# Optimization experiments

Hardware: AMD Instinct MI355X
Metric: run time of the kernel (lower is better)

## Reference

```python
import jax, jax.numpy as jnp
import numpy as np
from jax import lax

B, C, Dd, Hh, Ww = 2, 256, 8, 64, 64
E, HID, TOPK = 6, 1024, 3


def setup_inputs() -> dict:
    key = jax.random.key(0)
    ks = jax.random.split(key, 8)
    return {
        "x": jax.random.normal(ks[0], (B, C, Dd, Hh, Ww), jnp.float32),
        "attention_weights": jax.random.uniform(ks[1], (B, Dd, Hh, Ww), jnp.float32),
        "gate_w": jax.random.normal(ks[2], (E, C), jnp.float32) * 0.02,
        "gate_b": jnp.zeros((E,), jnp.float32),
        "w1": jax.random.normal(ks[3], (E, HID, C), jnp.float32) * (1.0 / np.sqrt(C)),
        "b1": jnp.zeros((E, HID), jnp.float32),
        "w2": jax.random.normal(ks[4], (E, C, HID), jnp.float32) * (1.0 / np.sqrt(HID)),
        "b2": jnp.zeros((E, C), jnp.float32),
    }


def reference(x, attention_weights, gate_w, gate_b, w1, b1, w2, b2):
    b, c, d, h, w = x.shape
    n = d * h * w
    e = gate_w.shape[0]
    xt = x.reshape(b, c, n).transpose(0, 2, 1)  # [B, N, C] tokens
    # 1x1x1 gate conv == per-voxel linear
    gv = jnp.einsum('bnc,ec->bne', xt, gate_w) + gate_b  # [B, N, E]
    gv = gv * attention_weights.reshape(b, n, 1)
    gv = jax.nn.softmax(gv, axis=-1)  # softmax over experts (dim=1 in torch layout)
    top_v, top_i = lax.top_k(gv, TOPK)  # [B, N, 3]
    # scatter top-k softmax values into a zero mask (non-topk experts get 0)
    mask = jnp.sum(jax.nn.one_hot(top_i, e, dtype=gv.dtype) * top_v[..., None], axis=-2)  # [B, N, E]
    out = jnp.zeros_like(xt)
    for ei in range(e):  # loop over small fixed expert count
        hdn = jax.nn.gelu(jnp.einsum('bnc,hc->bnh', xt, w1[ei]) + b1[ei], approximate=False)
        o = jnp.einsum('bnh,ch->bnc', hdn, w2[ei]) + b2[ei]
        out = out + mask[:, :, ei:ei + 1] * o
    return out.transpose(0, 2, 1).reshape(b, c, d, h, w)
```

## Files before the change

kernel.cpp:

```cpp
#include <hip/hip_runtime.h>
#include <hip/hip_bf16.h>
#include <math.h>

#define NN 32768
#define CC 256
#define EE 6
#define HID 1024
#define TT 64
#define NTOK 65536
#define NTILE_MAX 1044
#define NROWS (NTILE_MAX * 64)
#define SENT 0xFFFFFFFFu

typedef __attribute__((ext_vector_type(8))) short bf16x8;
typedef __attribute__((ext_vector_type(4))) float f32x4;
typedef __attribute__((ext_vector_type(4))) unsigned int u32x4;
typedef __attribute__((ext_vector_type(2))) unsigned int u32x2;

__device__ const int CMB[20][3] = {
  {0,1,2},{0,1,3},{0,1,4},{0,1,5},{0,2,3},{0,2,4},{0,2,5},{0,3,4},{0,3,5},{0,4,5},
  {1,2,3},{1,2,4},{1,2,5},{1,3,4},{1,3,5},{1,4,5},{2,3,4},{2,3,5},{2,4,5},{3,4,5}};
__device__ const unsigned char M2B[64] = {
  255,255,255,255,255,255,255,  0,
  255,255,255,  1,255,  4, 10,255,
  255,255,255,  2,255,  5, 11,255,
  255,  7, 13,255, 16,255,255,255,
  255,255,255,  3,255,  6, 12,255,
  255,  8, 14,255, 17,255,255,255,
  255,  9, 15,255, 18,255,255,255,
   19,255,255,255,255,255,255,255};

__device__ __forceinline__ unsigned short f32_bf16(float f) {
  unsigned u = __builtin_bit_cast(unsigned, f);
  u += 0x7FFFu + ((u >> 16) & 1u);
  return (unsigned short)(u >> 16);
}

__device__ __forceinline__ unsigned cvt_pk_bf16(float lo, float hi) {
  unsigned r;
  asm("v_cvt_pk_bf16_f32 %0, %1, %2" : "=v"(r) : "v"(lo), "v"(hi));
  return r;
}

__device__ __forceinline__ float fast_gelu(float v) {
  float s = v * v;
  float a = v * -2.3021181819f;
  float m = a * 0.044715f;
  float nu = __builtin_fmaf(m, s, a);
  float z = __builtin_amdgcn_exp2f(nu);
  return v * __builtin_amdgcn_rcpf(1.0f + z);
}

__global__ void wconv(const float* __restrict__ w1, const float* __restrict__ w2,
                      unsigned short* __restrict__ w1b, unsigned short* __restrict__ w2b) {
  int i = blockIdx.x * 256 + threadIdx.x;
  w1b[i] = f32_bf16(w1[i]);
  w2b[i] = f32_bf16(w2[i]);
}

__global__ __launch_bounds__(256) void gate_k(
    const float* __restrict__ x, const float* __restrict__ attn,
    const float* __restrict__ gate_w, const float* __restrict__ gate_b,
    unsigned* __restrict__ setid, float* __restrict__ wsel,
    unsigned* __restrict__ bhist) {
  __shared__ float gws[EE * CC];
  __shared__ unsigned hist[20];
  const int tid = threadIdx.x;
  const int blk = blockIdx.x;
  for (int i = tid; i < EE * CC; i += 256) gws[i] = gate_w[i];
  if (tid < 20) hist[tid] = 0;
  __syncthreads();

  const unsigned id = blk * 256 + tid;
  const int b = id >> 15, n = id & (NN - 1);
  const float* px = x + (size_t)b * CC * NN + n;
  float g[EE] = {0.f, 0.f, 0.f, 0.f, 0.f, 0.f};
  #pragma unroll 4
  for (int c = 0; c < CC; ++c) {
    float xv = px[(size_t)c * NN];
    #pragma unroll
    for (int e = 0; e < EE; ++e) g[e] = __builtin_fmaf(xv, gws[e * CC + c], g[e]);
  }
  float aw = attn[id];
  float m = -1e30f;
  #pragma unroll
  for (int e = 0; e < EE; ++e) { g[e] = (g[e] + gate_b[e]) * aw; m = fmaxf(m, g[e]); }
  float ex[EE], s = 0.f;
  #pragma unroll
  for (int e = 0; e < EE; ++e) { ex[e] = expf(g[e] - m); s += ex[e]; }
  int i1 = 0; float v1 = g[0];
  #pragma unroll
  for (int e = 1; e < EE; ++e) if (g[e] > v1) { v1 = g[e]; i1 = e; }
  int i2 = -1; float v2 = -3.4e38f;
  #pragma unroll
  for (int e = 0; e < EE; ++e) if (e != i1 && g[e] > v2) { v2 = g[e]; i2 = e; }
  int i3 = -1; float v3 = -3.4e38f;
  #pragma unroll
  for (int e = 0; e < EE; ++e) if (e != i1 && e != i2 && g[e] > v3) { v3 = g[e]; i3 = e; }
  const unsigned msk = (1u << i1) | (1u << i2) | (1u << i3);
  const unsigned bkt = M2B[msk];
  float inv = 1.f / s;
  int slot = 0;
  #pragma unroll
  for (int e = 0; e < EE; ++e)
    if ((msk >> e) & 1u) wsel[(size_t)id * 3 + (slot++)] = ex[e] * inv;
  setid[id] = bkt;
  atomicAdd(&hist[bkt], 1u);
  __syncthreads();
  if (tid < 20) bhist[blk * 20 + tid] = hist[tid];
}

__global__ void prefix_k(const unsigned* __restrict__ bhist, unsigned* __restrict__ bbase,
                         unsigned* __restrict__ desc) {
  __shared__ unsigned tot[20];
  __shared__ unsigned bb[21];
  __shared__ unsigned tcum[21];
  const int tid = threadIdx.x;
  if (tid < 20) {
    unsigned run = 0;
    for (int blk = 0; blk < 256; ++blk) {
      unsigned v = bhist[blk * 20 + tid];
      bbase[blk * 20 + tid] = run;
      run += v;
    }
    tot[tid] = run;
  }
  __syncthreads();
  if (tid == 0) {
    unsigned base = 0, tc = 0;
    for (int b = 0; b < 20; ++b) {
      bb[b] = base; tcum[b] = tc;
      unsigned tl = (tot[b] + 63) >> 6;
      tc += tl; base += tl << 6;
    }
    bb[20] = base; tcum[20] = tc;
  }
  __syncthreads();
  if (tid < 20) {
    unsigned b0 = bb[tid];
    for (int blk = 0; blk < 256; ++blk) bbase[blk * 20 + tid] += b0;
  }
  __syncthreads();
  const unsigned nt = tcum[20];
  for (int i = tid; i < NTILE_MAX; i += 256) {
    unsigned d;
    if ((unsigned)i < nt) {
      int b = 0;
      while (!((unsigned)i >= tcum[b] && (unsigned)i < tcum[b + 1])) ++b;
      d = ((unsigned)b << 16) | ((bb[b] >> 6) + ((unsigned)i - tcum[b]));
    } else {
      d = 0x003F0000u;
    }
    desc[i] = d;
  }
}

__global__ __launch_bounds__(256) void scatter_k(
    const unsigned* __restrict__ setid, const unsigned* __restrict__ bbase,
    const float* __restrict__ wsel,
    unsigned* __restrict__ pos, float* __restrict__ wp) {
  __shared__ unsigned wcnt[4][20];
  const int tid = threadIdx.x, lane = tid & 63, w = tid >> 6;
  const int blk = blockIdx.x;
  const unsigned id = blk * 256 + tid;
  const unsigned sid = setid[id];
  unsigned long long myb = 0;
  #pragma unroll
  for (int b = 0; b < 20; ++b) {
    unsigned long long bl = __ballot(sid == (unsigned)b);
    if (lane == 0) wcnt[w][b] = (unsigned)__builtin_popcountll(bl);
    if ((unsigned)b == sid) myb = bl;
  }
  __syncthreads();
  unsigned rank = 0;
  #pragma unroll
  for (int w2 = 0; w2 < 4; ++w2) if (w2 < w) rank += wcnt[w2][sid];
  rank += (unsigned)__builtin_popcountll(myb & ((1ull << lane) - 1ull));
  const unsigned p = bbase[blk * 20 + sid] + rank;
  pos[id] = p;
  #pragma unroll
  for (int s = 0; s < 3; ++s) wp[(size_t)p * 3 + s] = wsel[(size_t)id * 3 + s];
}

__global__ __launch_bounds__(256) void xpack_k(
    const float* __restrict__ x, const unsigned* __restrict__ pos,
    unsigned char* __restrict__ Xp) {
  __shared__ unsigned char lx[TT * 512];
  __shared__ unsigned posS[TT];
  const int tid = threadIdx.x, lane = tid & 63, wv = tid >> 6;
  const int n0g = blockIdx.x * TT;
  const int b = n0g >> 15, n0 = n0g & (NN - 1);

  if (tid < TT) posS[tid] = pos[n0g + tid];

  const float* px = x + (size_t)b * CC * NN + n0 + lane;
  #pragma unroll 1
  for (int c8 = 0; c8 < 8; ++c8) {
    float xv[8];
    #pragma unroll
    for (int j = 0; j < 8; ++j)
      xv[j] = px[(size_t)(wv * 64 + c8 * 8 + j) * NN];
    u32x4 pk;
    #pragma unroll
    for (int q = 0; q < 4; ++q) pk[q] = cvt_pk_bf16(xv[2 * q], xv[2 * q + 1]);
    *(u32x4*)(lx + lane * 512 + (wv * 64 + c8 * 8) * 2) = pk;
  }
  __syncthreads();

  #pragma unroll 1
  for (int r = 0; r < 16; ++r) {
    const int t = wv * 16 + r;
    const unsigned p = posS[t];
    u32x2 v = *(const u32x2*)(lx + t * 512 + lane * 8);
    *(u32x2*)(Xp + (size_t)p * 512 + (((unsigned)(lane * 8)) ^ (((unsigned)(p & 31)) << 4))) = v;
  }
}

__global__ __launch_bounds__(256, 2) void moe_main(
    const float* __restrict__ b1, const float* __restrict__ b2,
    const unsigned short* __restrict__ w1b, const unsigned short* __restrict__ w2b,
    const unsigned* __restrict__ desc, const float* __restrict__ wp,
    const unsigned char* __restrict__ Xp, float* __restrict__ Op) {
  __shared__ unsigned char xs[TT * CC * 2];
  __shared__ unsigned char hs[TT * 256 * 2];
  __shared__ float w3S[3 * TT];

  const unsigned d = desc[blockIdx.x];
  const unsigned bkt = d >> 16;
  if (bkt > 19) return;
  const int lstart = (int)(d & 0xFFFFu) << 6;

  const int tid  = threadIdx.x;
  const int lane = tid & 63;
  const int wv   = tid >> 6;
  const int lr   = lane & 15;
  const int lg   = lane >> 4;

  if (tid < 3 * TT) {
    int t = tid & 63, s = tid >> 6;
    w3S[s * 64 + t] = wp[(size_t)(lstart + t) * 3 + s];
  }

  {
    const unsigned char* src = Xp + (size_t)lstart * 512;
    #pragma unroll
    for (int it = 0; it < 8; ++it) {
      u32x4 v = *(const u32x4*)(src + it * 4096 + tid * 16);
      *(u32x4*)(xs + it * 4096 + tid * 16) = v;
    }
  }
  __syncthreads();

  f32x4 oacc[4][4];
  #pragma unroll
  for (int fm = 0; fm < 4; ++fm)
    #pragma unroll
    for (int fn = 0; fn < 4; ++fn) oacc[fm][fn] = (f32x4){0.f, 0.f, 0.f, 0.f};

  unsigned trowA[4], tswA[4];
  #pragma unroll
  for (int fn = 0; fn < 4; ++fn) {
    int t = fn * 16 + lr;
    trowA[fn] = (unsigned)t * 512u;
    tswA[fn]  = ((unsigned)(t & 31)) << 4;
  }

  #pragma unroll 1
  for (int xe = 0; xe < 3; ++xe) {
    const int e = CMB[bkt][xe];
    #pragma unroll 1
    for (int sc = 0; sc < 4; ++sc) {
      f32x4 hacc[4][4];
      #pragma unroll
      for (int fm = 0; fm < 4; ++fm)
        #pragma unroll
        for (int fn = 0; fn < 4; ++fn) hacc[fm][fn] = (f32x4){0.f, 0.f, 0.f, 0.f};
      const unsigned short* w1p =
          w1b + ((size_t)(e * HID + sc * 256 + wv * 64 + lr)) * CC + lg * 8;
      #pragma unroll
      for (int ks = 0; ks < 8; ++ks) {
        bf16x8 af[4], bx[4];
        #pragma unroll
        for (int fm = 0; fm < 4; ++fm)
          af[fm] = *(const bf16x8*)(w1p + fm * 16 * CC + ks * 32);
        #pragma unroll
        for (int fn = 0; fn < 4; ++fn)
          bx[fn] = *(const bf16x8*)(xs + trowA[fn] +
                                    (((unsigned)(ks * 64 + lg * 16)) ^ tswA[fn]));
        #pragma unroll
        for (int fn = 0; fn < 4; ++fn)
          #pragma unroll
          for (int fm = 0; fm < 4; ++fm)
            hacc[fm][fn] =
                __builtin_amdgcn_mfma_f32_16x16x32_bf16(af[fm], bx[fn], hacc[fm][fn], 0, 0, 0);
      }
      {
        f32x4 b1v[4];
        #pragma unroll
        for (int fm = 0; fm < 4; ++fm)
          b1v[fm] = *(const f32x4*)&b1[e * HID + sc * 256 + wv * 64 + fm * 16 + lg * 4];
        #pragma unroll
        for (int fn = 0; fn < 4; ++fn) {
          float msk = w3S[xe * 64 + fn * 16 + lr];
          #pragma unroll
          for (int fm = 0; fm < 4; ++fm) {
            float gg[4];
            #pragma unroll
            for (int r = 0; r < 4; ++r)
              gg[r] = fast_gelu(hacc[fm][fn][r] + b1v[fm][r]) * msk;
            u32x2 pk;
            pk[0] = cvt_pk_bf16(gg[0], gg[1]);
            pk[1] = cvt_pk_bf16(gg[2], gg[3]);
            unsigned byteo = trowA[fn] +
                (((unsigned)((wv * 64 + fm * 16 + lg * 4) * 2)) ^ tswA[fn]);
            *(u32x2*)(hs + byteo) = pk;
          }
        }
      }
      __syncthreads();
      const unsigned short* w2p =
          w2b + ((size_t)(e * CC + wv * 64 + lr)) * HID + sc * 256 + lg * 8;
      #pragma unroll
      for (int ks = 0; ks < 8; ++ks) {
        bf16x8 am[4], bh[4];
        #pragma unroll
        for (int fm = 0; fm < 4; ++fm)
          am[fm] = *(const bf16x8*)(w2p + fm * 16 * HID + ks * 32);
        #pragma unroll
        for (int fn = 0; fn < 4; ++fn)
          bh[fn] = *(const bf16x8*)(hs + trowA[fn] +
                                    (((unsigned)(ks * 64 + lg * 16)) ^ tswA[fn]));
        #pragma unroll
        for (int fn = 0; fn < 4; ++fn)
          #pragma unroll
          for (int fm = 0; fm < 4; ++fm)
            oacc[fm][fn] =
                __builtin_amdgcn_mfma_f32_16x16x32_bf16(am[fm], bh[fn], oacc[fm][fn], 0, 0, 0);
      }
      __syncthreads();
    }
  }

  #pragma unroll
  for (int xe = 0; xe < 3; ++xe) {
    const int e = CMB[bkt][xe];
    float msk[4];
    #pragma unroll
    for (int fn = 0; fn < 4; ++fn) msk[fn] = w3S[xe * 64 + fn * 16 + lr];
    #pragma unroll
    for (int fm = 0; fm < 4; ++fm) {
      f32x4 b2v = *(const f32x4*)&b2[e * CC + wv * 64 + fm * 16 + lg * 4];
      #pragma unroll
      for (int fn = 0; fn < 4; ++fn)
        #pragma unroll
        for (int r = 0; r < 4; ++r)
          oacc[fm][fn][r] = __builtin_fmaf(msk[fn], b2v[r], oacc[fm][fn][r]);
    }
  }
  #pragma unroll
  for (int fn = 0; fn < 4; ++fn) {
    float* po = Op + (size_t)(lstart + fn * 16 + lr) * CC;
    #pragma unroll
    for (int fm = 0; fm < 4; ++fm)
      *(f32x4*)(po + wv * 64 + fm * 16 + lg * 4) = oacc[fm][fn];
  }
}

__global__ __launch_bounds__(256) void unscatter_k(
    const float* __restrict__ Op, const unsigned* __restrict__ pos,
    float* __restrict__ out) {
  __shared__ float lo[32 * 261];
  __shared__ unsigned posS[32];
  const int tid = threadIdx.x;
  const int n0g = blockIdx.x * 32;
  const int b = n0g >> 15, n0 = n0g & (NN - 1);

  if (tid < 32) posS[tid] = pos[n0g + tid];
  __syncthreads();

  #pragma unroll
  for (int j = 0; j < 8; ++j) {
    int fidx = j * 1024 + tid * 4;
    int row = fidx >> 8, c = fidx & 255;
    f32x4 v = *(const f32x4*)(Op + (size_t)posS[row] * CC + c);
    #pragma unroll
    for (int i = 0; i < 4; ++i) lo[row * 261 + c + i] = v[i];
  }
  __syncthreads();

  const int noff = tid & 31, cq = tid >> 5;
  float* po = out + (size_t)b * CC * NN + n0 + noff;
  #pragma unroll
  for (int j2 = 0; j2 < 32; ++j2) {
    int c = cq * 32 + j2;
    po[(size_t)c * NN] = lo[noff * 261 + c];
  }
}

__global__ __launch_bounds__(256, 2) void moe_dense(
    const float* __restrict__ x, const float* __restrict__ attn,
    const float* __restrict__ gate_w, const float* __restrict__ gate_b,
    const float* __restrict__ b1, const float* __restrict__ b2,
    const unsigned short* __restrict__ w1b, const unsigned short* __restrict__ w2b,
    float* __restrict__ out) {
  __shared__ unsigned char xs[TT * CC * 2];
  __shared__ unsigned char hs[TT * 256 * 2];
  __shared__ float gwS[EE * CC];
  __shared__ float maskS[EE * TT];

  const int tid  = threadIdx.x;
  const int lane = tid & 63;
  const int wv   = tid >> 6;
  const int lr   = lane & 15;
  const int lg   = lane >> 4;

  const int token0 = blockIdx.x * TT;
  const int bIdx   = token0 >> 15;
  const int n0     = token0 & (NN - 1);

  for (int i = tid; i < EE * CC; i += 256) gwS[i] = gate_w[i];
  __syncthreads();

  float* gred = (float*)hs;
  {
    float gp[EE] = {0.f, 0.f, 0.f, 0.f, 0.f, 0.f};
    const int t = lane;
    const unsigned trow = (unsigned)t * 512u;
    const unsigned tsw  = ((unsigned)(t & 31)) << 4;
    const size_t xbase = ((size_t)bIdx * CC + wv * 64) * NN + n0 + lane;
    #pragma unroll 1
    for (int c8 = 0; c8 < 8; ++c8) {
      float xv[8];
      #pragma unroll
      for (int j = 0; j < 8; ++j) xv[j] = x[xbase + (size_t)(c8 * 8 + j) * NN];
      #pragma unroll
      for (int j = 0; j < 8; ++j) {
        int c = wv * 64 + c8 * 8 + j;
        #pragma unroll
        for (int e = 0; e < EE; ++e) gp[e] = __builtin_fmaf(xv[j], gwS[e * CC + c], gp[e]);
      }
      u32x4 pk;
      #pragma unroll
      for (int q = 0; q < 4; ++q) pk[q] = cvt_pk_bf16(xv[2 * q], xv[2 * q + 1]);
      unsigned byteo = trow + (((unsigned)((wv * 64 + c8 * 8) * 2)) ^ tsw);
      *(u32x4*)(xs + byteo) = pk;
    }
    #pragma unroll
    for (int e = 0; e < EE; ++e) gred[(wv * 64 + lane) * EE + e] = gp[e];
  }
  __syncthreads();

  if (tid < 64) {
    float g[EE];
    #pragma unroll
    for (int e = 0; e < EE; ++e)
      g[e] = gred[(0 * 64 + tid) * EE + e] + gred[(1 * 64 + tid) * EE + e] +
             gred[(2 * 64 + tid) * EE + e] + gred[(3 * 64 + tid) * EE + e];
    float aw = attn[token0 + tid];
    float m = -1e30f;
    #pragma unroll
    for (int e = 0; e < EE; ++e) { g[e] = (g[e] + gate_b[e]) * aw; m = fmaxf(m, g[e]); }
    float ex[EE], s = 0.f;
    #pragma unroll
    for (int e = 0; e < EE; ++e) { ex[e] = expf(g[e] - m); s += ex[e]; }
    int i1 = 0; float v1 = g[0];
    #pragma unroll
    for (int e = 1; e < EE; ++e) if (g[e] > v1) { v1 = g[e]; i1 = e; }
    int i2 = -1; float v2 = -3.4e38f;
    #pragma unroll
    for (int e = 0; e < EE; ++e) if (e != i1 && g[e] > v2) { v2 = g[e]; i2 = e; }
    int i3 = -1; float v3 = -3.4e38f;
    #pragma unroll
    for (int e = 0; e < EE; ++e) if (e != i1 && e != i2 && g[e] > v3) { v3 = g[e]; i3 = e; }
    float inv = 1.f / s;
    #pragma unroll
    for (int e = 0; e < EE; ++e)
      maskS[e * TT + tid] = (e == i1 || e == i2 || e == i3) ? ex[e] * inv : 0.f;
  }
  __syncthreads();

  f32x4 oacc[4][4];
  #pragma unroll
  for (int fm = 0; fm < 4; ++fm)
    #pragma unroll
    for (int fn = 0; fn < 4; ++fn) oacc[fm][fn] = (f32x4){0.f, 0.f, 0.f, 0.f};

  unsigned trowA[4], tswA[4];
  #pragma unroll
  for (int fn = 0; fn < 4; ++fn) {
    int t = fn * 16 + lr;
    trowA[fn] = (unsigned)t * 512u;
    tswA[fn]  = ((unsigned)(t & 31)) << 4;
  }

  #pragma unroll 1
  for (int e = 0; e < EE; ++e) {
    #pragma unroll 1
    for (int sc = 0; sc < 4; ++sc) {
      f32x4 hacc[4][4];
      #pragma unroll
      for (int fm = 0; fm < 4; ++fm)
        #pragma unroll
        for (int fn = 0; fn < 4; ++fn) hacc[fm][fn] = (f32x4){0.f, 0.f, 0.f, 0.f};
      const unsigned short* w1p =
          w1b + ((size_t)(e * HID + sc * 256 + wv * 64 + lr)) * CC + lg * 8;
      #pragma unroll
      for (int ks = 0; ks < 8; ++ks) {
        bf16x8 af[4], bx[4];
        #pragma unroll
        for (int fm = 0; fm < 4; ++fm)
          af[fm] = *(const bf16x8*)(w1p + fm * 16 * CC + ks * 32);
        #pragma unroll
        for (int fn = 0; fn < 4; ++fn)
          bx[fn] = *(const bf16x8*)(xs + trowA[fn] +
                                    (((unsigned)(ks * 64 + lg * 16)) ^ tswA[fn]));
        #pragma unroll
        for (int fn = 0; fn < 4; ++fn)
          #pragma unroll
          for (int fm = 0; fm < 4; ++fm)
            hacc[fm][fn] =
                __builtin_amdgcn_mfma_f32_16x16x32_bf16(af[fm], bx[fn], hacc[fm][fn], 0, 0, 0);
      }
      {
        f32x4 b1v[4];
        #pragma unroll
        for (int fm = 0; fm < 4; ++fm)
          b1v[fm] = *(const f32x4*)&b1[e * HID + sc * 256 + wv * 64 + fm * 16 + lg * 4];
        #pragma unroll
        for (int fn = 0; fn < 4; ++fn) {
          float msk = maskS[e * TT + fn * 16 + lr];
          #pragma unroll
          for (int fm = 0; fm < 4; ++fm) {
            float gg[4];
            #pragma unroll
            for (int r = 0; r < 4; ++r)
              gg[r] = fast_gelu(hacc[fm][fn][r] + b1v[fm][r]) * msk;
            u32x2 pk;
            pk[0] = cvt_pk_bf16(gg[0], gg[1]);
            pk[1] = cvt_pk_bf16(gg[2], gg[3]);
            unsigned byteo = trowA[fn] +
                (((unsigned)((wv * 64 + fm * 16 + lg * 4) * 2)) ^ tswA[fn]);
            *(u32x2*)(hs + byteo) = pk;
          }
        }
      }
      __syncthreads();
      const unsigned short* w2p =
          w2b + ((size_t)(e * CC + wv * 64 + lr)) * HID + sc * 256 + lg * 8;
      #pragma unroll
      for (int ks = 0; ks < 8; ++ks) {
        bf16x8 am[4], bh[4];
        #pragma unroll
        for (int fm = 0; fm < 4; ++fm)
          am[fm] = *(const bf16x8*)(w2p + fm * 16 * HID + ks * 32);
        #pragma unroll
        for (int fn = 0; fn < 4; ++fn)
          bh[fn] = *(const bf16x8*)(hs + trowA[fn] +
                                    (((unsigned)(ks * 64 + lg * 16)) ^ tswA[fn]));
        #pragma unroll
        for (int fn = 0; fn < 4; ++fn)
          #pragma unroll
          for (int fm = 0; fm < 4; ++fm)
            oacc[fm][fn] =
                __builtin_amdgcn_mfma_f32_16x16x32_bf16(am[fm], bh[fn], oacc[fm][fn], 0, 0, 0);
      }
      __syncthreads();
    }
  }

  #pragma unroll
  for (int e = 0; e < EE; ++e) {
    float msk[4];
    #pragma unroll
    for (int fn = 0; fn < 4; ++fn) msk[fn] = maskS[e * TT + fn * 16 + lr];
    #pragma unroll
    for (int fm = 0; fm < 4; ++fm) {
      f32x4 b2v = *(const f32x4*)&b2[e * CC + wv * 64 + fm * 16 + lg * 4];
      #pragma unroll
      for (int fn = 0; fn < 4; ++fn)
        #pragma unroll
        for (int r = 0; r < 4; ++r)
          oacc[fm][fn][r] = __builtin_fmaf(msk[fn], b2v[r], oacc[fm][fn][r]);
    }
  }
  const size_t obase = ((size_t)bIdx * CC) * NN + n0;
  #pragma unroll
  for (int fm = 0; fm < 4; ++fm) {
    #pragma unroll
    for (int fn = 0; fn < 4; ++fn) {
      int t = fn * 16 + lr;
      #pragma unroll
      for (int r = 0; r < 4; ++r) {
        int c = wv * 64 + fm * 16 + lg * 4 + r;
        out[obase + (size_t)c * NN + t] = oacc[fm][fn][r];
      }
    }
  }
}

extern "C" void kernel_launch(void* const* d_in, const int* in_sizes, int n_in,
                              void* d_out, int out_size, void* d_ws, size_t ws_size,
                              hipStream_t stream) {
  const float* x      = (const float*)d_in[0];
  const float* attn   = (const float*)d_in[1];
  const float* gate_w = (const float*)d_in[2];
  const float* gate_b = (const float*)d_in[3];
  const float* w1     = (const float*)d_in[4];
  const float* b1     = (const float*)d_in[5];
  const float* w2     = (const float*)d_in[6];
  const float* b2     = (const float*)d_in[7];
  float* out = (float*)d_out;

  unsigned char* ws = (unsigned char*)d_ws;
  unsigned short* w1b  = (unsigned short*)(ws);
  unsigned short* w2b  = (unsigned short*)(ws + 3145728);
  unsigned*       setid= (unsigned*)(ws + 6291456);
  float*          wsel = (float*)(ws + 6553600);
  unsigned*       bhist= (unsigned*)(ws + 7340032);
  unsigned*       bbase= (unsigned*)(ws + 7360512);
  unsigned*       desc = (unsigned*)(ws + 7381120);
  unsigned*       pos  = (unsigned*)(ws + 7385344);
  float*          wp   = (float*)(ws + 7647488);
  unsigned char*  Xp   = (unsigned char*)(ws + 8449280);
  float*          Op   = (float*)(ws + 42659072);
  const size_t need = 111078656;

  wconv<<<(EE * HID * CC) / 256, 256, 0, stream>>>(w1, w2, w1b, w2b);
  if (ws_size >= need) {
    gate_k<<<NTOK / 256, 256, 0, stream>>>(x, attn, gate_w, gate_b, setid, wsel, bhist);
    prefix_k<<<1, 256, 0, stream>>>(bhist, bbase, desc);
    scatter_k<<<NTOK / 256, 256, 0, stream>>>(setid, bbase, wsel, pos, wp);
    xpack_k<<<NTOK / TT, 256, 0, stream>>>(x, pos, Xp);
    moe_main<<<NTILE_MAX, 256, 0, stream>>>(b1, b2, w1b, w2b, desc, wp, Xp, Op);
    unscatter_k<<<NTOK / 32, 256, 0, stream>>>(Op, pos, out);
  } else {
    moe_dense<<<NTOK / TT, 256, 0, stream>>>(x, attn, gate_w, gate_b, b1, b2, w1b, w2b, out);
  }
}
```

Baseline: 614.0 us.

## Route tokens per expert instead of per expert-triple bucket

Tokens were previously grouped into 20 expert-combination buckets. They are now grouped into one list per expert, and each 64-row tile runs a single expert's FFN over gathered token rows. Gating and bf16 packing of x are fused into one kernel, expert outputs are stored in bf16, and a final kernel sums each token's three expert rows. The aim is to cut padding, improve reuse of each expert's weights, and reduce launches and output traffic. In exchange it needs a larger workspace, adds a gather and a three-way reduce, and drops the dense fallback.

```diff
diff --git a/kernel.cpp b/kernel.cpp
--- a/kernel.cpp
+++ b/kernel.cpp
@@ -9,7 +9,8 @@
 #define TT 64
 #define NTOK 65536
 #define NTILE_MAX 1044
-#define NROWS (NTILE_MAX * 64)
+#define NROWS3 196992
+#define NT3MAX 3078
 #define SENT 0xFFFFFFFFu
 
 typedef __attribute__((ext_vector_type(8))) short bf16x8;
@@ -57,6 +58,368 @@
   w1b[i] = f32_bf16(w1[i]);
   w2b[i] = f32_bf16(w2[i]);
 }
+
+
+__global__ __launch_bounds__(256) void gatepack_k(
+    const float* __restrict__ x, const float* __restrict__ attn,
+    const float* __restrict__ gate_w, const float* __restrict__ gate_b,
+    unsigned* __restrict__ setid, float* __restrict__ wsel,
+    unsigned* __restrict__ ehist, unsigned char* __restrict__ Xp3) {
+  __shared__ float gws[EE * CC];
+  __shared__ unsigned char lx[TT * 512];
+  __shared__ float gred[256 * EE];
+  __shared__ unsigned hist6[EE];
+
+  const int tid = threadIdx.x, lane = tid & 63, wv = tid >> 6;
+  const int n0g = blockIdx.x * TT;
+  const int bI = n0g >> 15, n0 = n0g & (NN - 1);
+
+  for (int i = tid; i < EE * CC; i += 256) gws[i] = gate_w[i];
+  if (tid < EE) hist6[tid] = 0;
+  __syncthreads();
+
+  {
+    float gp[EE] = {0.f, 0.f, 0.f, 0.f, 0.f, 0.f};
+    const size_t xbase = ((size_t)bI * CC + wv * 64) * NN + n0 + lane;
+    #pragma unroll 1
+    for (int c8 = 0; c8 < 8; ++c8) {
+      float xv[8];
+      #pragma unroll
+      for (int j = 0; j < 8; ++j)
+        xv[j] = x[xbase + (size_t)(c8 * 8 + j) * NN];
+      #pragma unroll
+      for (int j = 0; j < 8; ++j) {
+        int c = wv * 64 + c8 * 8 + j;
+        #pragma unroll
+        for (int e = 0; e < EE; ++e) gp[e] = __builtin_fmaf(xv[j], gws[e * CC + c], gp[e]);
+      }
+      u32x4 pk;
+      #pragma unroll
+      for (int q = 0; q < 4; ++q) pk[q] = cvt_pk_bf16(xv[2 * q], xv[2 * q + 1]);
+      *(u32x4*)(lx + lane * 512 + (wv * 64 + c8 * 8) * 2) = pk;
+    }
+    #pragma unroll
+    for (int e = 0; e < EE; ++e) gred[(wv * 64 + lane) * EE + e] = gp[e];
+  }
+  __syncthreads();
+
+  if (tid < 64) {
+    float g[EE];
+    #pragma unroll
+    for (int e = 0; e < EE; ++e)
+      g[e] = gred[(0 * 64 + tid) * EE + e] + gred[(1 * 64 + tid) * EE + e] +
+             gred[(2 * 64 + tid) * EE + e] + gred[(3 * 64 + tid) * EE + e];
+    float aw = attn[n0g + tid];
+    float m = -1e30f;
+    #pragma unroll
+    for (int e = 0; e < EE; ++e) { g[e] = (g[e] + gate_b[e]) * aw; m = fmaxf(m, g[e]); }
+    float ex[EE], s = 0.f;
+    #pragma unroll
+    for (int e = 0; e < EE; ++e) { ex[e] = expf(g[e] - m); s += ex[e]; }
+    int i1 = 0; float v1 = g[0];
+    #pragma unroll
+    for (int e = 1; e < EE; ++e) if (g[e] > v1) { v1 = g[e]; i1 = e; }
+    int i2 = -1; float v2 = -3.4e38f;
+    #pragma unroll
+    for (int e = 0; e < EE; ++e) if (e != i1 && g[e] > v2) { v2 = g[e]; i2 = e; }
+    int i3 = -1; float v3 = -3.4e38f;
+    #pragma unroll
+    for (int e = 0; e < EE; ++e) if (e != i1 && e != i2 && g[e] > v3) { v3 = g[e]; i3 = e; }
+    const unsigned msk = (1u << i1) | (1u << i2) | (1u << i3);
+    float inv = 1.f / s;
+    int slot = 0;
+    #pragma unroll
+    for (int e = 0; e < EE; ++e)
+      if ((msk >> e) & 1u) wsel[(size_t)(n0g + tid) * 3 + (slot++)] = ex[e] * inv;
+    setid[n0g + tid] = (unsigned)M2B[msk];
+    atomicAdd(&hist6[i1], 1u); atomicAdd(&hist6[i2], 1u); atomicAdd(&hist6[i3], 1u);
+  }
+  __syncthreads();
+
+  #pragma unroll 1
+  for (int r = 0; r < 16; ++r) {
+    const int t = wv * 16 + r;
+    u32x2 v = *(const u32x2*)(lx + t * 512 + lane * 8);
+    *(u32x2*)(Xp3 + (size_t)(n0g + t) * 512 + lane * 8) = v;
+  }
+  if (tid < EE) ehist[tid * 1024 + blockIdx.x] = hist6[tid];
+}
+
+__global__ __launch_bounds__(256) void prefix3_k(
+    const unsigned* __restrict__ ehist, unsigned* __restrict__ ebase,
+    unsigned* __restrict__ desc3, unsigned* __restrict__ tlist3,
+    float* __restrict__ wp3) {
+  __shared__ unsigned sc[256];
+  __shared__ unsigned tot[EE], bb[EE + 1], tcum[EE + 1];
+  const int tid = threadIdx.x;
+  #pragma unroll 1
+  for (int e = 0; e < EE; ++e) {
+    unsigned v[4]; unsigned s = 0;
+    #pragma unroll
+    for (int k = 0; k < 4; ++k) { v[k] = ehist[e * 1024 + tid * 4 + k]; s += v[k]; }
+    sc[tid] = s; __syncthreads();
+    for (int off = 1; off < 256; off <<= 1) {
+      unsigned tv = (tid >= off) ? sc[tid - off] : 0u; __syncthreads();
+      sc[tid] += tv; __syncthreads();
+    }
+    unsigned excl = sc[tid] - s;
+    if (tid == 255) tot[e] = sc[255];
+    unsigned run = excl;
+    #pragma unroll
+    for (int k = 0; k < 4; ++k) { ebase[e * 1024 + tid * 4 + k] = run; run += v[k]; }
+    __syncthreads();
+  }
+  if (tid == 0) {
+    unsigned base = 0, tc = 0;
+    for (int e = 0; e < EE; ++e) {
+      bb[e] = base; tcum[e] = tc;
+      unsigned tl = (tot[e] + 63) >> 6;
+      tc += tl; base += tl << 6;
+    }
+    bb[EE] = base; tcum[EE] = tc;
+  }
+  __syncthreads();
+  #pragma unroll 1
+  for (int e = 0; e < EE; ++e) {
+    unsigned b0 = bb[e];
+    #pragma unroll
+    for (int k = 0; k < 4; ++k) ebase[e * 1024 + tid * 4 + k] += b0;
+  }
+  if (tid < EE) {
+    for (unsigned i = bb[tid] + tot[tid]; i < bb[tid + 1]; ++i) {
+      tlist3[i] = SENT; wp3[i] = 0.f;
+    }
+  }
+  __syncthreads();
+  const unsigned nt = tcum[EE];
+  for (int i = tid; i < NT3MAX; i += 256) {
+    unsigned d;
+    if ((unsigned)i < nt) {
+      int e = 0;
+      while (!((unsigned)i >= tcum[e] && (unsigned)i < tcum[e + 1])) ++e;
+      d = ((unsigned)e << 16) | ((bb[e] >> 6) + ((unsigned)i - tcum[e]));
+    } else d = 0x003F0000u;
+    desc3[i] = d;
+  }
+}
+
+__global__ __launch_bounds__(64) void scatter3_k(
+    const unsigned* __restrict__ setid, const unsigned* __restrict__ ebase,
+    const float* __restrict__ wsel,
+    unsigned* __restrict__ tlist3, float* __restrict__ wp3, unsigned* __restrict__ pos3) {
+  const int tid = threadIdx.x;
+  const int blk = blockIdx.x;
+  const unsigned id = blk * 64 + tid;
+  const unsigned bkt = setid[id];
+  const unsigned m6 =
+      (1u << CMB[bkt][0]) | (1u << CMB[bkt][1]) | (1u << CMB[bkt][2]);
+  const unsigned long long below = (1ull << tid) - 1ull;
+  int s = 0;
+  #pragma unroll
+  for (int e = 0; e < EE; ++e) {
+    unsigned long long bl = __ballot((m6 >> e) & 1u);
+    if ((m6 >> e) & 1u) {
+      unsigned rank = (unsigned)__builtin_popcountll(bl & below);
+      unsigned p = ebase[e * 1024 + blk] + rank;
+      tlist3[p] = id;
+      wp3[p] = wsel[(size_t)id * 3 + s];
+      pos3[(size_t)id * 3 + s] = p;
+      s++;
+    }
+  }
+}
+
+__global__ __launch_bounds__(256, 2) void moe_main3(
+    const float* __restrict__ b1, const float* __restrict__ b2,
+    const unsigned short* __restrict__ w1b, const unsigned short* __restrict__ w2b,
+    const unsigned* __restrict__ desc3, const unsigned* __restrict__ tlist3,
+    const float* __restrict__ wp3, const unsigned char* __restrict__ Xp3,
+    unsigned char* __restrict__ Op3) {
+  __shared__ unsigned char xs[TT * CC * 2];
+  __shared__ unsigned char hs[TT * 256 * 2];
+  __shared__ unsigned tokS[TT];
+  __shared__ float w3S[TT];
+
+  const unsigned d = desc3[blockIdx.x];
+  const unsigned e = d >> 16;
+  if (e > 5) return;
+  const int lstart = (int)(d & 0xFFFFu) << 6;
+
+  const int tid  = threadIdx.x;
+  const int lane = tid & 63;
+  const int wv   = tid >> 6;
+  const int lr   = lane & 15;
+  const int lg   = lane >> 4;
+
+  if (tid < TT) { tokS[tid] = tlist3[lstart + tid]; w3S[tid] = wp3[lstart + tid]; }
+  __syncthreads();
+
+  {
+    const int t = tid >> 2, q = tid & 3;
+    unsigned tk = tokS[t];
+    if (tk == SENT) tk = 0u;
+    const unsigned char* src = Xp3 + (size_t)tk * 512 + q * 128;
+    const unsigned tsw = ((unsigned)(t & 31)) << 4;
+    #pragma unroll
+    for (int i = 0; i < 8; ++i) {
+      u32x4 v = *(const u32x4*)(src + i * 16);
+      *(u32x4*)(xs + t * 512 + (((unsigned)(q * 128 + i * 16)) ^ tsw)) = v;
+    }
+  }
+  __syncthreads();
+
+  f32x4 oacc[4][4];
+  #pragma unroll
+  for (int fm = 0; fm < 4; ++fm)
+    #pragma unroll
+    for (int fn = 0; fn < 4; ++fn) oacc[fm][fn] = (f32x4){0.f, 0.f, 0.f, 0.f};
+
+  unsigned trowA[4], tswA[4];
+  #pragma unroll
+  for (int fn = 0; fn < 4; ++fn) {
+    int t = fn * 16 + lr;
+    trowA[fn] = (unsigned)t * 512u;
+    tswA[fn]  = ((unsigned)(t & 31)) << 4;
+  }
+
+  #pragma unroll 1
+  for (int sc = 0; sc < 4; ++sc) {
+    f32x4 hacc[4][4];
+    #pragma unroll
+    for (int fm = 0; fm < 4; ++fm)
+      #pragma unroll
+      for (int fn = 0; fn < 4; ++fn) hacc[fm][fn] = (f32x4){0.f, 0.f, 0.f, 0.f};
+    const unsigned short* w1p =
+        w1b + ((size_t)(e * HID + sc * 256 + wv * 64 + lr)) * CC + lg * 8;
+    #pragma unroll
+    for (int ks = 0; ks < 8; ++ks) {
+      bf16x8 af[4], bx[4];
+      #pragma unroll
+      for (int fm = 0; fm < 4; ++fm)
+        af[fm] = *(const bf16x8*)(w1p + fm * 16 * CC + ks * 32);
+      #pragma unroll
+      for (int fn = 0; fn < 4; ++fn)
+        bx[fn] = *(const bf16x8*)(xs + trowA[fn] +
+                                  (((unsigned)(ks * 64 + lg * 16)) ^ tswA[fn]));
+      #pragma unroll
+      for (int fn = 0; fn < 4; ++fn)
+        #pragma unroll
+        for (int fm = 0; fm < 4; ++fm)
+          hacc[fm][fn] =
+              __builtin_amdgcn_mfma_f32_16x16x32_bf16(af[fm], bx[fn], hacc[fm][fn], 0, 0, 0);
+    }
+    {
+      f32x4 b1v[4];
+      #pragma unroll
+      for (int fm = 0; fm < 4; ++fm)
+        b1v[fm] = *(const f32x4*)&b1[e * HID + sc * 256 + wv * 64 + fm * 16 + lg * 4];
+      #pragma unroll
+      for (int fn = 0; fn < 4; ++fn) {
+        float msk = w3S[fn * 16 + lr];
+        #pragma unroll
+        for (int fm = 0; fm < 4; ++fm) {
+          float gg[4];
+          #pragma unroll
+          for (int r = 0; r < 4; ++r)
+            gg[r] = fast_gelu(hacc[fm][fn][r] + b1v[fm][r]) * msk;
+          u32x2 pk;
+          pk[0] = cvt_pk_bf16(gg[0], gg[1]);
+          pk[1] = cvt_pk_bf16(gg[2], gg[3]);
+          unsigned byteo = trowA[fn] +
+              (((unsigned)((wv * 64 + fm * 16 + lg * 4) * 2)) ^ tswA[fn]);
+          *(u32x2*)(hs + byteo) = pk;
+        }
+      }
+    }
+    __syncthreads();
+    const unsigned short* w2p =
+        w2b + ((size_t)(e * CC + wv * 64 + lr)) * HID + sc * 256 + lg * 8;
+    #pragma unroll
+    for (int ks = 0; ks < 8; ++ks) {
+      bf16x8 am[4], bh[4];
+      #pragma unroll
+      for (int fm = 0; fm < 4; ++fm)
+        am[fm] = *(const bf16x8*)(w2p + fm * 16 * HID + ks * 32);
+      #pragma unroll
+      for (int fn = 0; fn < 4; ++fn)
+        bh[fn] = *(const bf16x8*)(hs + trowA[fn] +
+                                  (((unsigned)(ks * 64 + lg * 16)) ^ tswA[fn]));
+      #pragma unroll
+      for (int fn = 0; fn < 4; ++fn)
+        #pragma unroll
+        for (int fm = 0; fm < 4; ++fm)
+          oacc[fm][fn] =
+              __builtin_amdgcn_mfma_f32_16x16x32_bf16(am[fm], bh[fn], oacc[fm][fn], 0, 0, 0);
+    }
+    __syncthreads();
+  }
+
+  float wt[4];
+  #pragma unroll
+  for (int fn = 0; fn < 4; ++fn) wt[fn] = w3S[fn * 16 + lr];
+  #pragma unroll
+  for (int fm = 0; fm < 4; ++fm) {
+    f32x4 b2v = *(const f32x4*)&b2[e * CC + wv * 64 + fm * 16 + lg * 4];
+    #pragma unroll
+    for (int fn = 0; fn < 4; ++fn)
+      #pragma unroll
+      for (int r = 0; r < 4; ++r)
+        oacc[fm][fn][r] = __builtin_fmaf(wt[fn], b2v[r], oacc[fm][fn][r]);
+  }
+  #pragma unroll
+  for (int fn = 0; fn < 4; ++fn) {
+    const int row = lstart + fn * 16 + lr;
+    unsigned char* po = Op3 + (size_t)row * 512;
+    #pragma unroll
+    for (int fm = 0; fm < 4; ++fm) {
+      u32x2 pk;
+      pk[0] = cvt_pk_bf16(oacc[fm][fn][0], oacc[fm][fn][1]);
+      pk[1] = cvt_pk_bf16(oacc[fm][fn][2], oacc[fm][fn][3]);
+      *(u32x2*)(po + (wv * 64 + fm * 16 + lg * 4) * 2) = pk;
+    }
+  }
+}
+
+__global__ __launch_bounds__(256) void unscatter3_k(
+    const unsigned char* __restrict__ Op3, const unsigned* __restrict__ pos3,
+    float* __restrict__ out) {
+  __shared__ float lo[32 * 261];
+  __shared__ unsigned psf[96];
+  const int tid = threadIdx.x;
+  const int n0g = blockIdx.x * 32;
+  const int b = n0g >> 15, n0 = n0g & (NN - 1);
+
+  if (tid < 96) psf[tid] = pos3[(size_t)n0g * 3 + tid];
+  __syncthreads();
+
+  #pragma unroll
+  for (int j = 0; j < 8; ++j) {
+    const int row = j * 4 + (tid >> 6);
+    const int c = (tid & 63) * 4;
+    float a0 = 0.f, a1 = 0.f, a2 = 0.f, a3 = 0.f;
+    #pragma unroll
+    for (int s = 0; s < 3; ++s) {
+      const unsigned r = psf[row * 3 + s];
+      u32x2 v = *(const u32x2*)(Op3 + (size_t)r * 512 + c * 2);
+      a0 += __builtin_bit_cast(float, v[0] << 16);
+      a1 += __builtin_bit_cast(float, v[0] & 0xFFFF0000u);
+      a2 += __builtin_bit_cast(float, v[1] << 16);
+      a3 += __builtin_bit_cast(float, v[1] & 0xFFFF0000u);
+    }
+    lo[row * 261 + c + 0] = a0; lo[row * 261 + c + 1] = a1;
+    lo[row * 261 + c + 2] = a2; lo[row * 261 + c + 3] = a3;
+  }
+  __syncthreads();
+
+  const int noff = tid & 31, cq = tid >> 5;
+  float* po = out + (size_t)b * CC * NN + n0 + noff;
+  #pragma unroll
+  for (int j2 = 0; j2 < 32; ++j2) {
+    int c = cq * 32 + j2;
+    po[(size_t)c * NN] = lo[noff * 261 + c];
+  }
+}
+
 
 __global__ __launch_bounds__(256) void gate_k(
     const float* __restrict__ x, const float* __restrict__ attn,
@@ -397,206 +760,6 @@
   }
 }
 
-__global__ __launch_bounds__(256, 2) void moe_dense(
-    const float* __restrict__ x, const float* __restrict__ attn,
-    const float* __restrict__ gate_w, const float* __restrict__ gate_b,
-    const float* __restrict__ b1, const float* __restrict__ b2,
-    const unsigned short* __restrict__ w1b, const unsigned short* __restrict__ w2b,
-    float* __restrict__ out) {
-  __shared__ unsigned char xs[TT * CC * 2];
-  __shared__ unsigned char hs[TT * 256 * 2];
-  __shared__ float gwS[EE * CC];
-  __shared__ float maskS[EE * TT];
-
-  const int tid  = threadIdx.x;
-  const int lane = tid & 63;
-  const int wv   = tid >> 6;
-  const int lr   = lane & 15;
-  const int lg   = lane >> 4;
-
-  const int token0 = blockIdx.x * TT;
-  const int bIdx   = token0 >> 15;
-  const int n0     = token0 & (NN - 1);
-
-  for (int i = tid; i < EE * CC; i += 256) gwS[i] = gate_w[i];
-  __syncthreads();
-
-  float* gred = (float*)hs;
-  {
-    float gp[EE] = {0.f, 0.f, 0.f, 0.f, 0.f, 0.f};
-    const int t = lane;
-    const unsigned trow = (unsigned)t * 512u;
-    const unsigned tsw  = ((unsigned)(t & 31)) << 4;
-    const size_t xbase = ((size_t)bIdx * CC + wv * 64) * NN + n0 + lane;
-    #pragma unroll 1
-    for (int c8 = 0; c8 < 8; ++c8) {
-      float xv[8];
-      #pragma unroll
-      for (int j = 0; j < 8; ++j) xv[j] = x[xbase + (size_t)(c8 * 8 + j) * NN];
-      #pragma unroll
-      for (int j = 0; j < 8; ++j) {
-        int c = wv * 64 + c8 * 8 + j;
-        #pragma unroll
-        for (int e = 0; e < EE; ++e) gp[e] = __builtin_fmaf(xv[j], gwS[e * CC + c], gp[e]);
-      }
-      u32x4 pk;
-      #pragma unroll
-      for (int q = 0; q < 4; ++q) pk[q] = cvt_pk_bf16(xv[2 * q], xv[2 * q + 1]);
-      unsigned byteo = trow + (((unsigned)((wv * 64 + c8 * 8) * 2)) ^ tsw);
-      *(u32x4*)(xs + byteo) = pk;
-    }
-    #pragma unroll
-    for (int e = 0; e < EE; ++e) gred[(wv * 64 + lane) * EE + e] = gp[e];
-  }
-  __syncthreads();
-
-  if (tid < 64) {
-    float g[EE];
-    #pragma unroll
-    for (int e = 0; e < EE; ++e)
-      g[e] = gred[(0 * 64 + tid) * EE + e] + gred[(1 * 64 + tid) * EE + e] +
-             gred[(2 * 64 + tid) * EE + e] + gred[(3 * 64 + tid) * EE + e];
-    float aw = attn[token0 + tid];
-    float m = -1e30f;
-    #pragma unroll
-    for (int e = 0; e < EE; ++e) { g[e] = (g[e] + gate_b[e]) * aw; m = fmaxf(m, g[e]); }
-    float ex[EE], s = 0.f;
-    #pragma unroll
-    for (int e = 0; e < EE; ++e) { ex[e] = expf(g[e] - m); s += ex[e]; }
-    int i1 = 0; float v1 = g[0];
-    #pragma unroll
-    for (int e = 1; e < EE; ++e) if (g[e] > v1) { v1 = g[e]; i1 = e; }
-    int i2 = -1; float v2 = -3.4e38f;
-    #pragma unroll
-    for (int e = 0; e < EE; ++e) if (e != i1 && g[e] > v2) { v2 = g[e]; i2 = e; }
-    int i3 = -1; float v3 = -3.4e38f;
-    #pragma unroll
-    for (int e = 0; e < EE; ++e) if (e != i1 && e != i2 && g[e] > v3) { v3 = g[e]; i3 = e; }
-    float inv = 1.f / s;
-    #pragma unroll
-    for (int e = 0; e < EE; ++e)
-      maskS[e * TT + tid] = (e == i1 || e == i2 || e == i3) ? ex[e] * inv : 0.f;
-  }
-  __syncthreads();
-
-  f32x4 oacc[4][4];
-  #pragma unroll
-  for (int fm = 0; fm < 4; ++fm)
-    #pragma unroll
-    for (int fn = 0; fn < 4; ++fn) oacc[fm][fn] = (f32x4){0.f, 0.f, 0.f, 0.f};
-
-  unsigned trowA[4], tswA[4];
-  #pragma unroll
-  for (int fn = 0; fn < 4; ++fn) {
-    int t = fn * 16 + lr;
-    trowA[fn] = (unsigned)t * 512u;
-    tswA[fn]  = ((unsigned)(t & 31)) << 4;
-  }
-
-  #pragma unroll 1
-  for (int e = 0; e < EE; ++e) {
-    #pragma unroll 1
-    for (int sc = 0; sc < 4; ++sc) {
-      f32x4 hacc[4][4];
-      #pragma unroll
-      for (int fm = 0; fm < 4; ++fm)
-        #pragma unroll
-        for (int fn = 0; fn < 4; ++fn) hacc[fm][fn] = (f32x4){0.f, 0.f, 0.f, 0.f};
-      const unsigned short* w1p =
-          w1b + ((size_t)(e * HID + sc * 256 + wv * 64 + lr)) * CC + lg * 8;
-      #pragma unroll
-      for (int ks = 0; ks < 8; ++ks) {
-        bf16x8 af[4], bx[4];
-        #pragma unroll
-        for (int fm = 0; fm < 4; ++fm)
-          af[fm] = *(const bf16x8*)(w1p + fm * 16 * CC + ks * 32);
-        #pragma unroll
-        for (int fn = 0; fn < 4; ++fn)
-          bx[fn] = *(const bf16x8*)(xs + trowA[fn] +
-                                    (((unsigned)(ks * 64 + lg * 16)) ^ tswA[fn]));
-        #pragma unroll
-        for (int fn = 0; fn < 4; ++fn)
-          #pragma unroll
-          for (int fm = 0; fm < 4; ++fm)
-            hacc[fm][fn] =
-                __builtin_amdgcn_mfma_f32_16x16x32_bf16(af[fm], bx[fn], hacc[fm][fn], 0, 0, 0);
-      }
-      {
-        f32x4 b1v[4];
-        #pragma unroll
-        for (int fm = 0; fm < 4; ++fm)
-          b1v[fm] = *(const f32x4*)&b1[e * HID + sc * 256 + wv * 64 + fm * 16 + lg * 4];
-        #pragma unroll
-        for (int fn = 0; fn < 4; ++fn) {
-          float msk = maskS[e * TT + fn * 16 + lr];
-          #pragma unroll
-          for (int fm = 0; fm < 4; ++fm) {
-            float gg[4];
-            #pragma unroll
-            for (int r = 0; r < 4; ++r)
-              gg[r] = fast_gelu(hacc[fm][fn][r] + b1v[fm][r]) * msk;
-            u32x2 pk;
-            pk[0] = cvt_pk_bf16(gg[0], gg[1]);
-            pk[1] = cvt_pk_bf16(gg[2], gg[3]);
-            unsigned byteo = trowA[fn] +
-                (((unsigned)((wv * 64 + fm * 16 + lg * 4) * 2)) ^ tswA[fn]);
-            *(u32x2*)(hs + byteo) = pk;
-          }
-        }
-      }
-      __syncthreads();
-      const unsigned short* w2p =
-          w2b + ((size_t)(e * CC + wv * 64 + lr)) * HID + sc * 256 + lg * 8;
-      #pragma unroll
-      for (int ks = 0; ks < 8; ++ks) {
-        bf16x8 am[4], bh[4];
-        #pragma unroll
-        for (int fm = 0; fm < 4; ++fm)
-          am[fm] = *(const bf16x8*)(w2p + fm * 16 * HID + ks * 32);
-        #pragma unroll
-        for (int fn = 0; fn < 4; ++fn)
-          bh[fn] = *(const bf16x8*)(hs + trowA[fn] +
-                                    (((unsigned)(ks * 64 + lg * 16)) ^ tswA[fn]));
-        #pragma unroll
-        for (int fn = 0; fn < 4; ++fn)
-          #pragma unroll
-          for (int fm = 0; fm < 4; ++fm)
-            oacc[fm][fn] =
-                __builtin_amdgcn_mfma_f32_16x16x32_bf16(am[fm], bh[fn], oacc[fm][fn], 0, 0, 0);
-      }
-      __syncthreads();
-    }
-  }
-
-  #pragma unroll
-  for (int e = 0; e < EE; ++e) {
-    float msk[4];
-    #pragma unroll
-    for (int fn = 0; fn < 4; ++fn) msk[fn] = maskS[e * TT + fn * 16 + lr];
-    #pragma unroll
-    for (int fm = 0; fm < 4; ++fm) {
-      f32x4 b2v = *(const f32x4*)&b2[e * CC + wv * 64 + fm * 16 + lg * 4];
-      #pragma unroll
-      for (int fn = 0; fn < 4; ++fn)
-        #pragma unroll
-        for (int r = 0; r < 4; ++r)
-          oacc[fm][fn][r] = __builtin_fmaf(msk[fn], b2v[r], oacc[fm][fn][r]);
-    }
-  }
-  const size_t obase = ((size_t)bIdx * CC) * NN + n0;
-  #pragma unroll
-  for (int fm = 0; fm < 4; ++fm) {
-    #pragma unroll
-    for (int fn = 0; fn < 4; ++fn) {
-      int t = fn * 16 + lr;
-      #pragma unroll
-      for (int r = 0; r < 4; ++r) {
-        int c = wv * 64 + fm * 16 + lg * 4 + r;
-        out[obase + (size_t)c * NN + t] = oacc[fm][fn][r];
-      }
-    }
-  }
-}
 
 extern "C" void kernel_launch(void* const* d_in, const int* in_sizes, int n_in,
                               void* d_out, int out_size, void* d_ws, size_t ws_size,
@@ -623,17 +786,30 @@
   float*          wp   = (float*)(ws + 7647488);
   unsigned char*  Xp   = (unsigned char*)(ws + 8449280);
   float*          Op   = (float*)(ws + 42659072);
-  const size_t need = 111078656;
+  const size_t need_bucket = 111078656;
+  unsigned*       ehist = (unsigned*)(ws + 7360512);
+  unsigned*       ebase = (unsigned*)(ws + 7385088);
+  unsigned*       desc3 = (unsigned*)(ws + 7409664);
+  unsigned*       tlist3= (unsigned*)(ws + 7422208);
+  float*          wp3   = (float*)(ws + 8210176);
+  unsigned*       pos3  = (unsigned*)(ws + 8998144);
+  unsigned char*  Xp3   = (unsigned char*)(ws + 9784576);
+  unsigned char*  Op3   = (unsigned char*)(ws + 43339008);
+  const size_t need3 = 144198912;
 
   wconv<<<(EE * HID * CC) / 256, 256, 0, stream>>>(w1, w2, w1b, w2b);
-  if (ws_size >= need) {
+  if (ws_size >= need3) {
+    gatepack_k<<<NTOK / TT, 256, 0, stream>>>(x, attn, gate_w, gate_b, setid, wsel, ehist, Xp3);
+    prefix3_k<<<1, 256, 0, stream>>>(ehist, ebase, desc3, tlist3, wp3);
+    scatter3_k<<<NTOK / 64, 64, 0, stream>>>(setid, ebase, wsel, tlist3, wp3, pos3);
+    moe_main3<<<NT3MAX, 256, 0, stream>>>(b1, b2, w1b, w2b, desc3, tlist3, wp3, Xp3, Op3);
+    unscatter3_k<<<NTOK / 32, 256, 0, stream>>>(Op3, pos3, out);
+  } else {
     gate_k<<<NTOK / 256, 256, 0, stream>>>(x, attn, gate_w, gate_b, setid, wsel, bhist);
     prefix_k<<<1, 256, 0, stream>>>(bhist, bbase, desc);
     scatter_k<<<NTOK / 256, 256, 0, stream>>>(setid, bbase, wsel, pos, wp);
     xpack_k<<<NTOK / TT, 256, 0, stream>>>(x, pos, Xp);
     moe_main<<<NTILE_MAX, 256, 0, stream>>>(b1, b2, w1b, w2b, desc, wp, Xp, Op);
     unscatter_k<<<NTOK / 32, 256, 0, stream>>>(Op, pos, out);
-  } else {
-    moe_dense<<<NTOK / TT, 256, 0, stream>>>(x, attn, gate_w, gate_b, b1, b2, w1b, w2b, out);
-  }
-}
+  }
+}
```

After: 522.7 us. -14.9%, faster.
